# Performance work log

Hardware: AMD Instinct MI355X
Metric: run time of the kernel (lower is better)

The kernel has to match this reference:

```python
import jax, jax.numpy as jnp
import numpy as np

B = 16           # number of graphs
H = 8            # heads
NC = 9           # num_coeffs = (lmax+1)^2
DM = 128         # d_model (sphere_channels)
F = NC * DM      # flat_dim = 1152
HD = F // H      # head_dim = 144
RD = 16          # rope_dim
EPS = 1e-5


def setup_inputs() -> dict:
    key = jax.random.key(0)
    ks = jax.random.split(key, 8)
    N = 8192
    x_emb = jax.random.normal(ks[0], (N, NC, DM), dtype=jnp.float32)
    batch = jnp.sort(jax.random.randint(ks[1], (N,), 0, B)).astype(jnp.int32)
    pos = jax.random.normal(ks[2], (N, 3), dtype=jnp.float32) * 3.0
    Wqkv = jax.random.normal(ks[3], (F, 3 * F), dtype=jnp.float32) / np.sqrt(F)
    Wout = jax.random.normal(ks[4], (F, F), dtype=jnp.float32) / np.sqrt(F)
    rope_freqs = jax.random.normal(ks[5], (RD,), dtype=jnp.float32) * 0.1
    Wrope = jax.random.normal(ks[6], (RD, H), dtype=jnp.float32) / np.sqrt(RD)
    gamma = jnp.ones((F,), dtype=jnp.float32)
    beta = jnp.zeros((F,), dtype=jnp.float32)
    return {"x_emb": x_emb, "pos": pos, "Wqkv": Wqkv, "Wout": Wout,
            "rope_freqs": rope_freqs, "Wrope": Wrope,
            "gamma": gamma, "beta": beta, "batch": batch}


def _pad_layout(batch, N):
    # sorted batch ids -> per-node rank within its graph, sizes per graph
    sizes = jnp.bincount(batch, length=B)                       # [B]
    offsets = jnp.concatenate([jnp.zeros((1,), sizes.dtype), jnp.cumsum(sizes)[:-1]])
    rank = jnp.arange(N, dtype=sizes.dtype) - offsets[batch]    # [N]
    n_max = int(np.asarray(jax.device_get(sizes)).max())        # concrete pad width
    return sizes, rank, n_max


def reference(x_emb, pos, Wqkv, Wout, rope_freqs, Wrope, gamma, beta, batch):
    N = x_emb.shape[0]
    x_flat = x_emb.reshape(N, F)
    sizes, rank, n_max = _pad_layout(batch, N)

    # dense padding  [B, N_max, *]; mask True = padding slot
    x_pad = jnp.zeros((B, n_max, F), x_flat.dtype).at[batch, rank].set(x_flat)
    pos_pad = jnp.zeros((B, n_max, 3), pos.dtype).at[batch, rank].set(pos)
    mask = jnp.arange(n_max)[None, :] >= sizes[:, None]         # [B, N_max]

    qkv = x_pad @ Wqkv                                          # [B, N_max, 3F]
    q, k, v = jnp.split(qkv, 3, axis=-1)
    def heads(t):
        return t.reshape(B, n_max, H, HD).transpose(0, 2, 1, 3)  # [B,H,N_max,HD]
    q, k, v = heads(q), heads(k), heads(v)

    scale = HD ** (-0.5)
    attn = jnp.einsum('bhid,bhjd->bhij', q, k) * scale          # [B,H,N,N]

    # Fourier distance bias
    diff = pos_pad[:, :, None, :] - pos_pad[:, None, :, :]      # [B,N,N,3]
    dist = jnp.linalg.norm(diff, axis=-1)                       # [B,N,N]
    fourier = jnp.cos(dist[..., None] * jnp.abs(rope_freqs))    # [B,N,N,RD]
    bias = jnp.einsum('bijr,rh->bhij', fourier, Wrope)          # [B,H,N,N]
    pad_mask = mask[:, None, :] | mask[:, :, None]              # [B,N,N]
    bias = jnp.where(pad_mask[:, None, :, :], 0.0, bias)
    attn = attn + bias

    attn = jnp.where(mask[:, None, None, :], -jnp.inf, attn)    # key mask
    attn = jax.nn.softmax(attn, axis=-1)
    attn = jnp.nan_to_num(attn)

    out = jnp.einsum('bhij,bhjd->bhid', attn, v)                # [B,H,N,HD]
    out = out.transpose(0, 2, 1, 3).reshape(B, n_max, F) @ Wout
    out_flat = out[batch, rank]                                 # gather back [N,F]

    h = x_flat + out_flat
    mu = jnp.mean(h, axis=-1, keepdims=True)
    var = jnp.var(h, axis=-1, keepdims=True)
    y = (h - mu) / jnp.sqrt(var + EPS) * gamma + beta
    return y.reshape(N, NC, DM)
```

## Files before the change

### kernel.cpp

```cpp
#include <hip/hip_runtime.h>

typedef unsigned short u16;
typedef unsigned int   u32;
typedef __attribute__((ext_vector_type(8)))  __bf16 bf16x8;
typedef __attribute__((ext_vector_type(4)))  float  f32x4;
typedef __attribute__((ext_vector_type(16))) float  f32x16;
typedef __attribute__((ext_vector_type(4)))  u32    u32x4;

#define F_DIM   1152
#define QKV_DIM 3456
#define HD_SCALE 0.083333333333333333f
#define LOG2E    1.4426950408889634f
#define KSC      (HD_SCALE*LOG2E)
#define MAX4    80

static __device__ __forceinline__ u16 f2bf(float f){
    u32 u = __builtin_bit_cast(u32, f);
    u32 r = u + 0x7fffu + ((u >> 16) & 1u);
    return (u16)(r >> 16);
}
static __device__ __forceinline__ u32 cvtpk(float lo, float hi){
    u32 r;
    asm("v_cvt_pk_bf16_f32 %0, %1, %2" : "=v"(r) : "v"(lo), "v"(hi));
    return r;
}

typedef __attribute__((address_space(1))) void gvoid;
typedef __attribute__((address_space(3))) void lvoid;
static __device__ __forceinline__ void gload16(const u16* g, u16* l){
    __builtin_amdgcn_global_load_lds((gvoid*)g, (lvoid*)l, 16, 0, 0);
}

__global__ __launch_bounds__(256) void prep_kernel(
        const float* __restrict__ x, u16* __restrict__ xb, int nCast, int n4,
        const float* __restrict__ Wqkv, u16* __restrict__ wqkvT,
        const float* __restrict__ Wout, u16* __restrict__ woutT,
        const int* __restrict__ batch, int* __restrict__ meta, int N){
    __shared__ float tile[32][33];
    const int b = blockIdx.x, t = threadIdx.x;
    const int T1 = (QKV_DIM/32)*(F_DIM/32);
    const int T2 = (F_DIM/32)*(F_DIM/32);
    if (b < nCast){
        int i = b*256 + t;
        if (i < n4){
            float4 v = ((const float4*)x)[i];
            ((ushort4*)xb)[i] = make_ushort4(f2bf(v.x), f2bf(v.y), f2bf(v.z), f2bf(v.w));
        }
        return;
    }
    if (b < nCast + T1 + T2){
        const float* in; u16* out; int R, C, bi;
        if (b < nCast + T1){ in = Wqkv; out = wqkvT; R = F_DIM; C = QKV_DIM; bi = b - nCast; }
        else               { in = Wout; out = woutT; R = F_DIM; C = F_DIM;  bi = b - nCast - T1; }
        int gx = C/32;
        int c0 = (bi % gx)*32, r0 = (bi / gx)*32;
        int tx = t & 31, ty = t >> 5;
        #pragma unroll
        for (int yy = ty; yy < 32; yy += 8)
            tile[yy][tx] = in[(size_t)(r0+yy)*C + (c0+tx)];
        __syncthreads();
        #pragma unroll
        for (int yy = ty; yy < 32; yy += 8)
            out[(size_t)(c0+yy)*R + (r0+tx)] = f2bf(tile[tx][yy]);
        return;
    }
    if (t <= 16){
        int lo = 0, hi = N;
        while (lo < hi){ int mid = (lo+hi)>>1; if (batch[mid] < t) lo = mid+1; else hi = mid; }
        meta[1+t] = lo;
    }
    __syncthreads();
    if (t == 0){
        int ps = 0, bcnt = 0, cnt4 = 0;
        for (int g = 0; g < 16; g++){
            int ng = meta[2+g] - meta[1+g];
            meta[20+g] = ps;
            meta[40+g] = bcnt;
            int nt = (ng + 31) / 32;
            ps += nt * 32;
            bcnt += nt * nt;
            int nt4 = (nt + 3) / 4;
            for (int q4 = 0; q4 < nt4; q4++){
                meta[64 + cnt4] = g;
                meta[64 + MAX4 + cnt4] = q4;
                cnt4++;
            }
        }
        meta[36] = ps;
        meta[56] = bcnt;
        meta[0]  = cnt4;
    }
}

template<bool OUT_BF16>
__global__ __launch_bounds__(512, 2) void gemm256(const u16* __restrict__ A,
                                                  const u16* __restrict__ Bt,
                                                  void* __restrict__ Cp,
                                                  int M, int Ncols, int K){
    __shared__ u16 sA[4][8192];
    __shared__ u16 sB[4][8192];
    const int nwg = gridDim.x;
    int orig = blockIdx.x;
    int qq = nwg >> 3, rr = nwg & 7;
    int xcd = orig & 7, pos = orig >> 3;
    int nid = (xcd < rr ? xcd*(qq+1) : rr*(qq+1) + (xcd-rr)*qq) + pos;
    const int gx = M >> 8;
    const int bm = (nid % gx) << 8, bn = (nid / gx) << 8;

    const int tid = threadIdx.x;
    const int w = tid >> 6, lane = tid & 63;
    const int wr = w >> 2, wc = w & 3;
    const int fr = lane & 15, fq = lane >> 4;
    const int swz8 = (fq ^ ((fr >> 1) & 3)) * 8;

    const u16* aS[2]; const u16* bS[2]; int dOf[2];
    #pragma unroll
    for (int p = 0; p < 2; p++){
        int idx = p*512 + tid;
        int row = idx >> 2, c = idx & 3;
        int sc = c ^ ((row >> 1) & 3);
        int brow = bn + row; if (brow > Ncols-1) brow = Ncols-1;
        aS[p] = A  + (size_t)(bm + row)*K + sc*8;
        bS[p] = Bt + (size_t)brow*K + sc*8;
        dOf[p] = idx*8;
    }

    f32x4 acc[8][4];
    #pragma unroll
    for (int m = 0; m < 8; m++)
        #pragma unroll
        for (int n = 0; n < 4; n++)
            #pragma unroll
            for (int e = 0; e < 4; e++) acc[m][n][e] = 0.f;

    const int nk = K >> 5;
    #pragma unroll
    for (int p = 0; p < 2; p++){ gload16(aS[p], &sA[0][dOf[p]]); gload16(bS[p], &sB[0][dOf[p]]); }
    #pragma unroll
    for (int p = 0; p < 2; p++){ gload16(aS[p]+32, &sA[1][dOf[p]]); gload16(bS[p]+32, &sB[1][dOf[p]]); }

    #pragma unroll 1
    for (int t = 0; t < nk; t++){
        int tp = (t+2 < nk) ? t+2 : nk-1;
        int bufS = (t+2) & 3;
        #pragma unroll
        for (int p = 0; p < 2; p++){
            gload16(aS[p] + tp*32, &sA[bufS][dOf[p]]);
            gload16(bS[p] + tp*32, &sB[bufS][dOf[p]]);
        }
        asm volatile("s_waitcnt vmcnt(8)\n\ts_barrier" ::: "memory");

        const u16* sAc = &sA[t & 3][0];
        const u16* sBc = &sB[t & 3][0];
        bf16x8 af[8], bfr[4];
        #pragma unroll
        for (int m = 0; m < 8; m++)
            af[m] = *(const bf16x8*)(sAc + (wr*128 + m*16 + fr)*32 + swz8);
        #pragma unroll
        for (int n = 0; n < 4; n++)
            bfr[n] = *(const bf16x8*)(sBc + (wc*64 + n*16 + fr)*32 + swz8);
        __builtin_amdgcn_s_setprio(1);
        #pragma unroll
        for (int m = 0; m < 8; m++)
            #pragma unroll
            for (int n = 0; n < 4; n++)
                acc[m][n] = __builtin_amdgcn_mfma_f32_16x16x32_bf16(af[m], bfr[n], acc[m][n], 0, 0, 0);
        __builtin_amdgcn_s_setprio(0);
    }

    #pragma unroll
    for (int m = 0; m < 8; m++)
        #pragma unroll
        for (int n = 0; n < 4; n++)
            #pragma unroll
            for (int r = 0; r < 4; r++){
                int row = bm + wr*128 + m*16 + fq*4 + r;
                int col = bn + wc*64 + n*16 + fr;
                if (col < Ncols){
                    float v = acc[m][n][r];
                    if (OUT_BF16) ((u16*)Cp)[(size_t)row*Ncols + col] = f2bf(v);
                    else          ((float*)Cp)[(size_t)row*Ncols + col] = v;
                }
            }
}

__global__ __launch_bounds__(256) void pack_v(const u16* __restrict__ qkv,
                                              u16* __restrict__ Vpack,
                                              const int* __restrict__ batch,
                                              const int* __restrict__ meta,
                                              int PT){
    __shared__ u16 tile[32][33];
    int nt0 = blockIdx.x*32, dt0 = blockIdx.y*32, h = blockIdx.z;
    int tx = threadIdx.x & 31, ty = threadIdx.x >> 5;
    #pragma unroll
    for (int yy = ty; yy < 32; yy += 8){
        int node = nt0+yy, d = dt0+tx;
        tile[yy][tx] = (d < 144) ? qkv[(size_t)node*QKV_DIM + 2*F_DIM + h*144 + d] : (u16)0;
    }
    __syncthreads();
    int node = nt0 + tx;
    int g = batch[node];
    int col = meta[20+g] + (node - meta[1+g]);
    int pt = col >> 5, cl = col & 31;
    #pragma unroll
    for (int yy = ty; yy < 32; yy += 8){
        int d = dt0+yy;
        if (d < 144) Vpack[(((size_t)h*PT + pt)*144 + d)*32 + cl] = tile[tx][yy];
    }
}

__global__ __launch_bounds__(256) void bias_kernel(const float* __restrict__ pos,
                                                   const float* __restrict__ rfreq,
                                                   const float* __restrict__ Wrope,
                                                   const int* __restrict__ meta,
                                                   u16* __restrict__ biasP){
    float absf[16], w[16][8];
    #pragma unroll
    for (int r = 0; r < 16; r++){
        absf[r] = fabsf(rfreq[r]);
        #pragma unroll
        for (int h = 0; h < 8; h++) w[r][h] = Wrope[r*8 + h] * LOG2E;
    }
    const int total = meta[56];
    const int t = threadIdx.x;
    for (int bb = blockIdx.x; bb < total; bb += gridDim.x){
        int g = 0;
        while (meta[40 + g + 1] <= bb) g++;
        int rem  = bb - meta[40 + g];
        int goff = meta[1+g];
        int ng   = meta[2+g] - goff;
        int ntg  = (ng + 31) >> 5;
        int qt   = rem / ntg;
        int jt   = rem - qt*ntg;
        size_t base = (size_t)bb * 8192;
        #pragma unroll
        for (int pp = 0; pp < 4; pp++){
            int p = t + pp*256;
            int i = p >> 5, c = p & 31;
            int p4 = c & 15;
            int j  = (p4 & 3) + ((p4 >> 2) << 3) + ((c >> 4) << 2);
            int qn = goff + qt*32 + i;  if (qn >= goff + ng) qn = goff + ng - 1;
            int kn = goff + jt*32 + j;  if (kn >= goff + ng) kn = goff + ng - 1;
            float dx = pos[qn*3+0] - pos[kn*3+0];
            float dy = pos[qn*3+1] - pos[kn*3+1];
            float dz = pos[qn*3+2] - pos[kn*3+2];
            float d  = sqrtf(dx*dx + dy*dy + dz*dz);
            float b[8];
            #pragma unroll
            for (int h = 0; h < 8; h++) b[h] = 0.f;
            #pragma unroll
            for (int r = 0; r < 16; r++){
                float cs = __cosf(d * absf[r]);
                #pragma unroll
                for (int h = 0; h < 8; h++) b[h] = fmaf(cs, w[r][h], b[h]);
            }
            #pragma unroll
            for (int h = 0; h < 8; h++)
                biasP[base + h*1024 + p] = f2bf(b[h]);
        }
    }
}

__global__ __launch_bounds__(256) void attn_kernel(
        const u16* __restrict__ qkv, const u16* __restrict__ Vpack,
        const u16* __restrict__ biasP, u16* __restrict__ attn_out,
        const int* __restrict__ meta, int PT){
    __shared__ u16 sK[2][10240];
    __shared__ u16 sV[2][10240];
    const int h = blockIdx.x & 7, t4 = blockIdx.x >> 3;
    if (t4 >= meta[0]) return;
    const int g    = meta[64 + t4];
    const int q4   = meta[64 + MAX4 + t4];
    const int goff = meta[1+g], gend = meta[2+g];
    const int ng   = gend - goff;
    const int ntg  = (ng + 31) >> 5;
    const int nt2  = (ntg + 1) >> 1;
    const int pst  = meta[20+g];
    const int boffg= meta[40+g];

    const int tid = threadIdx.x;
    const int w = tid >> 6, lane = tid & 63;
    const int li = lane & 31, hi = lane >> 5;
    const int qt = q4*4 + w;
    const int qbase = goff + qt*32;
    const int qtP = (qt < ntg) ? qt : (ntg - 1);

    int kOff[5];
    #pragma unroll
    for (int p = 0; p < 5; p++){
        int idx = p*256 + tid;
        if (idx > 1215) idx = 1215;
        int row = idx/19, c = idx - row*19;
        if (c == 18) c = 0;
        kOff[p] = row*QKV_DIM + c*8;
    }
    const u16* kBase = qkv + (size_t)goff*QKV_DIM + F_DIM + h*144;
    int vOff[5];
    #pragma unroll
    for (int p = 0; p < 5; p++){
        int idx = p*256 + tid;
        if (idx > 1151) idx = 1151;
        int tt = idx/576, i = idx - tt*576;
        int d = i >> 2, c = i & 3;
        vOff[p] = tt*4608 + d*32 + ((c ^ (d & 3)) << 3);
    }
    const u16* vBase = Vpack + ((size_t)h*PT + (pst >> 5))*4608;
    const u16* bBase = biasP + ((size_t)boffg + (size_t)qtP*ntg)*8192 + h*1024 + li*32 + hi*16;

    int qnode = qbase + li; if (qnode >= gend) qnode = gend - 1;
    const u16* qrow = qkv + (size_t)qnode*QKV_DIM + h*144;
    bf16x8 qf[9];
    #pragma unroll
    for (int kk = 0; kk < 9; kk++) qf[kk] = *(const bf16x8*)(qrow + kk*16 + hi*8);

    int jlr[16];
    #pragma unroll
    for (int r = 0; r < 16; r++) jlr[r] = (r & 3) + ((r >> 2) << 3) + (hi << 2);

    float lrun = 0.f;
    f32x16 O[5];
    #pragma unroll
    for (int dt = 0; dt < 5; dt++)
        #pragma unroll
        for (int e = 0; e < 16; e++) O[dt][e] = 0.f;

    u32x4 bA0, bA1, bA2, bA3, bN0, bN1, bN2, bN3;
    {
        int j1 = (ntg > 1) ? 1 : 0;
        bA0 = *(const u32x4*)bBase;
        bA1 = *(const u32x4*)(bBase + 8);
        bA2 = *(const u32x4*)(bBase + (size_t)j1*8192);
        bA3 = *(const u32x4*)(bBase + (size_t)j1*8192 + 8);
        #pragma unroll
        for (int p = 0; p < 5; p++) gload16(kBase + kOff[p], &sK[0][tid*8 + p*2048]);
        #pragma unroll
        for (int p = 0; p < 5; p++) gload16(vBase + vOff[p], &sV[0][tid*8 + p*2048]);
    }
    __syncthreads();

    #pragma unroll 1
    for (int t2 = 0; t2 < nt2; t2++){
        const int cur = t2 & 1;
        int jn0 = 2*t2+2; if (jn0 > ntg-1) jn0 = ntg-1;
        int jn1 = 2*t2+3; if (jn1 > ntg-1) jn1 = ntg-1;
        bN0 = *(const u32x4*)(bBase + (size_t)jn0*8192);
        bN1 = *(const u32x4*)(bBase + (size_t)jn0*8192 + 8);
        bN2 = *(const u32x4*)(bBase + (size_t)jn1*8192);
        bN3 = *(const u32x4*)(bBase + (size_t)jn1*8192 + 8);
        __builtin_amdgcn_sched_barrier(0);
        if (t2+1 < nt2){
            const u16* kb = kBase + (size_t)(t2+1)*64*QKV_DIM;
            const u16* vb = vBase + (size_t)(t2+1)*9216;
            #pragma unroll
            for (int p = 0; p < 5; p++) gload16(kb + kOff[p], &sK[cur^1][tid*8 + p*2048]);
            #pragma unroll
            for (int p = 0; p < 5; p++) gload16(vb + vOff[p], &sV[cur^1][tid*8 + p*2048]);
        }

        const u16* sKc = &sK[cur][0];
        f32x16 saccA, saccB;
        #pragma unroll
        for (int e = 0; e < 16; e++){ saccA[e] = 0.f; saccB[e] = 0.f; }
        __builtin_amdgcn_s_setprio(1);
        #pragma unroll
        for (int kk = 0; kk < 9; kk++){
            bf16x8 kfA = *(const bf16x8*)(sKc + li*152 + kk*16 + hi*8);
            bf16x8 kfB = *(const bf16x8*)(sKc + (32+li)*152 + kk*16 + hi*8);
            saccA = __builtin_amdgcn_mfma_f32_32x32x16_bf16(kfA, qf[kk], saccA, 0, 0, 0);
            saccB = __builtin_amdgcn_mfma_f32_32x32x16_bf16(kfB, qf[kk], saccB, 0, 0, 0);
        }
        __builtin_amdgcn_s_setprio(0);

        float bfA[16], bfB[16];
        #pragma unroll
        for (int q = 0; q < 4; q++){
            bfA[2*q]     = __builtin_bit_cast(float, bA0[q] << 16);
            bfA[2*q+1]   = __builtin_bit_cast(float, bA0[q] & 0xffff0000u);
            bfA[8+2*q]   = __builtin_bit_cast(float, bA1[q] << 16);
            bfA[8+2*q+1] = __builtin_bit_cast(float, bA1[q] & 0xffff0000u);
            bfB[2*q]     = __builtin_bit_cast(float, bA2[q] << 16);
            bfB[2*q+1]   = __builtin_bit_cast(float, bA2[q] & 0xffff0000u);
            bfB[8+2*q]   = __builtin_bit_cast(float, bA3[q] << 16);
            bfB[8+2*q+1] = __builtin_bit_cast(float, bA3[q] & 0xffff0000u);
        }

        const int j0 = t2*64;
        float pA[16], pB[16];
        float psum = 0.f;
        if (j0 + 64 <= ng){
            #pragma unroll
            for (int r = 0; r < 16; r++){
                float sA_ = fminf(fmaf(saccA[r], KSC, bfA[r]), 86.f);
                float sB_ = fminf(fmaf(saccB[r], KSC, bfB[r]), 86.f);
                pA[r] = exp2f(sA_); pB[r] = exp2f(sB_);
                psum += pA[r] + pB[r];
            }
        } else {
            #pragma unroll
            for (int r = 0; r < 16; r++){
                float sA_ = fminf(fmaf(saccA[r], KSC, bfA[r]), 86.f);
                float sB_ = fminf(fmaf(saccB[r], KSC, bfB[r]), 86.f);
                pA[r] = (j0 + jlr[r]      < ng) ? exp2f(sA_) : 0.f;
                pB[r] = (j0 + 32 + jlr[r] < ng) ? exp2f(sB_) : 0.f;
                psum += pA[r] + pB[r];
            }
        }
        psum += __shfl_xor(psum, 32);
        lrun += psum;

        u32 cA[8], oA[8], cB[8], oB[8];
        #pragma unroll
        for (int q = 0; q < 8; q++){ cA[q] = cvtpk(pA[2*q], pA[2*q+1]);
                                     cB[q] = cvtpk(pB[2*q], pB[2*q+1]); }
        #pragma unroll
        for (int q = 0; q < 8; q++){ oA[q] = (u32)__shfl_xor((int)cA[q], 32);
                                     oB[q] = (u32)__shfl_xor((int)cB[q], 32); }
        u32x4 a0, a1, b0, b1;
        if (hi == 0){
            a0[0]=cA[0]; a0[1]=cA[1]; a0[2]=oA[0]; a0[3]=oA[1];
            a1[0]=cA[4]; a1[1]=cA[5]; a1[2]=oA[4]; a1[3]=oA[5];
            b0[0]=cB[0]; b0[1]=cB[1]; b0[2]=oB[0]; b0[3]=oB[1];
            b1[0]=cB[4]; b1[1]=cB[5]; b1[2]=oB[4]; b1[3]=oB[5];
        } else {
            a0[0]=oA[2]; a0[1]=oA[3]; a0[2]=cA[2]; a0[3]=cA[3];
            a1[0]=oA[6]; a1[1]=oA[7]; a1[2]=cA[6]; a1[3]=cA[7];
            b0[0]=oB[2]; b0[1]=oB[3]; b0[2]=cB[2]; b0[3]=cB[3];
            b1[0]=oB[6]; b1[1]=oB[7]; b1[2]=cB[6]; b1[3]=cB[7];
        }
        bf16x8 pafA0 = __builtin_bit_cast(bf16x8, a0);
        bf16x8 pafA1 = __builtin_bit_cast(bf16x8, a1);
        bf16x8 pafB0 = __builtin_bit_cast(bf16x8, b0);
        bf16x8 pafB1 = __builtin_bit_cast(bf16x8, b1);

        const u16* sVc = &sV[cur][0];
        __builtin_amdgcn_s_setprio(1);
        #pragma unroll
        for (int dt = 0; dt < 5; dt++){
            int d = dt*32 + li;
            int dc = (d > 143) ? 143 : d;
            int swzlo = ((hi     ^ (dc & 3)) << 3);
            int swzhi = (((2+hi) ^ (dc & 3)) << 3);
            bf16x8 vA0 = *(const bf16x8*)(sVc + dc*32 + swzlo);
            bf16x8 vA1 = *(const bf16x8*)(sVc + dc*32 + swzhi);
            bf16x8 vB0 = *(const bf16x8*)(sVc + 4608 + dc*32 + swzlo);
            bf16x8 vB1 = *(const bf16x8*)(sVc + 4608 + dc*32 + swzhi);
            O[dt] = __builtin_amdgcn_mfma_f32_32x32x16_bf16(pafA0, vA0, O[dt], 0, 0, 0);
            O[dt] = __builtin_amdgcn_mfma_f32_32x32x16_bf16(pafA1, vA1, O[dt], 0, 0, 0);
            O[dt] = __builtin_amdgcn_mfma_f32_32x32x16_bf16(pafB0, vB0, O[dt], 0, 0, 0);
            O[dt] = __builtin_amdgcn_mfma_f32_32x32x16_bf16(pafB1, vB1, O[dt], 0, 0, 0);
        }
        __builtin_amdgcn_s_setprio(0);

        bA0 = bN0; bA1 = bN1; bA2 = bN2; bA3 = bN3;
        __syncthreads();
    }

    if (qt < ntg){
        float lr[16];
        #pragma unroll
        for (int r = 0; r < 16; r++) lr[r] = 1.0f / __shfl(lrun, jlr[r]);
        #pragma unroll
        for (int dt = 0; dt < 5; dt++){
            int d = dt*32 + li;
            if (d < 144){
                #pragma unroll
                for (int r = 0; r < 16; r++){
                    int qi = jlr[r];
                    if (qt*32 + qi < ng)
                        attn_out[(size_t)(qbase + qi)*F_DIM + h*144 + d] = f2bf(O[dt][r]*lr[r]);
                }
            }
        }
    }
}

__global__ __launch_bounds__(256) void ln_kernel(const float* __restrict__ x,
                                                 float* __restrict__ io,
                                                 const float* __restrict__ gamma,
                                                 const float* __restrict__ beta){
    const int node = blockIdx.x;
    const float* xr = x  + (size_t)node*F_DIM;
    float* yr       = io + (size_t)node*F_DIM;
    const int t = threadIdx.x;
    float h[5]; float s = 0.f, ss = 0.f;
    #pragma unroll
    for (int i = 0; i < 5; i++){
        int idx = t + i*256;
        float v = 0.f;
        if (idx < F_DIM) v = xr[idx] + yr[idx];
        h[i] = v; s += v; ss += v*v;
    }
    #pragma unroll
    for (int o = 32; o > 0; o >>= 1){ s += __shfl_down(s, o); ss += __shfl_down(ss, o); }
    __shared__ float rs[4], rss[4];
    __shared__ float smu, srstd;
    if ((t & 63) == 0){ rs[t>>6] = s; rss[t>>6] = ss; }
    __syncthreads();
    if (t == 0){
        float S  = rs[0]+rs[1]+rs[2]+rs[3];
        float SS = rss[0]+rss[1]+rss[2]+rss[3];
        float mu = S * (1.f/F_DIM);
        float var = SS * (1.f/F_DIM) - mu*mu;
        smu = mu; srstd = rsqrtf(var + 1e-5f);
    }
    __syncthreads();
    float mu = smu, rstd = srstd;
    #pragma unroll
    for (int i = 0; i < 5; i++){
        int idx = t + i*256;
        if (idx < F_DIM) yr[idx] = (h[i]-mu)*rstd*gamma[idx] + beta[idx];
    }
}

extern "C" void kernel_launch(void* const* d_in, const int* in_sizes, int n_in,
                              void* d_out, int out_size, void* d_ws, size_t ws_size,
                              hipStream_t stream){
    const float* x     = (const float*)d_in[0];
    const float* pos   = (const float*)d_in[1];
    const float* Wqkv  = (const float*)d_in[2];
    const float* Wout  = (const float*)d_in[3];
    const float* rfreq = (const float*)d_in[4];
    const float* Wrope = (const float*)d_in[5];
    const float* gamma = (const float*)d_in[6];
    const float* beta  = (const float*)d_in[7];
    const int*   batch = (const int*)d_in[8];

    const int N  = in_sizes[0] / F_DIM;
    const int PN = N + 512;
    const int PT = PN / 32;

    char* ws = (char*)d_ws;
    size_t off = 0;
    auto alloc = [&](size_t b){ size_t o = off; off += (b + 255) & ~(size_t)255; return o; };
    int* meta   = (int*)(ws + alloc((size_t)(64 + 2*MAX4 + 64)*sizeof(int)));
    u16* xb     = (u16*)(ws + alloc((size_t)N*F_DIM*2));
    u16* wqkvT  = (u16*)(ws + alloc((size_t)QKV_DIM*F_DIM*2));
    u16* woutT  = (u16*)(ws + alloc((size_t)F_DIM*F_DIM*2));
    u16* qkv    = (u16*)(ws + alloc((size_t)N*QKV_DIM*2));
    u16* Vpack  = (u16*)(ws + alloc((size_t)8*PT*144*32*2));
    u16* biasb  = (u16*)(ws + off);
    (void)ws_size; (void)n_in; (void)out_size;

    const int n4    = N*F_DIM/4;
    const int nCast = (n4 + 255)/256;
    const int nT    = (QKV_DIM/32)*(F_DIM/32) + (F_DIM/32)*(F_DIM/32);
    hipLaunchKernelGGL(prep_kernel, dim3(nCast + nT + 1), dim3(256), 0, stream,
                       x, xb, nCast, n4, Wqkv, wqkvT, Wout, woutT, batch, meta, N);
    hipLaunchKernelGGL((gemm256<true>), dim3((N/256)*((QKV_DIM+255)/256)), dim3(512), 0, stream,
                       xb, wqkvT, (void*)qkv, N, QKV_DIM, F_DIM);
    hipLaunchKernelGGL(pack_v, dim3(N/32, 5, 8), dim3(256), 0, stream,
                       qkv, Vpack, batch, meta, PT);
    hipLaunchKernelGGL(bias_kernel, dim3(2048), dim3(256), 0, stream,
                       pos, rfreq, Wrope, meta, biasb);
    hipLaunchKernelGGL(attn_kernel, dim3(MAX4*8), dim3(256), 0, stream,
                       qkv, Vpack, biasb, xb, meta, PT);
    hipLaunchKernelGGL((gemm256<false>), dim3((N/256)*((F_DIM+255)/256)), dim3(512), 0, stream,
                       xb, woutT, d_out, N, F_DIM, F_DIM);
    hipLaunchKernelGGL(ln_kernel, dim3(N), dim3(256), 0, stream,
                       x, (float*)d_out, gamma, beta);
}
```

Before: 301.2 us.

## Fuse bias computation into prep kernel and halve attention key tile

Moves the Fourier distance bias computation into the prep kernel as an extra 2048 blocks, which recompute graph offsets locally, and removes the separate bias launch. The bias work then runs alongside the cast and transpose work. The attention kernel now processes one 32-key tile per iteration instead of two, which shrinks shared memory and registers to allow higher occupancy. The trade-off is more loop iterations and barriers per key and less MFMA work between syncs.

```diff
diff --git a/kernel.cpp b/kernel.cpp
--- a/kernel.cpp
+++ b/kernel.cpp
@@ -13,6 +13,7 @@
 #define LOG2E    1.4426950408889634f
 #define KSC      (HD_SCALE*LOG2E)
 #define MAX4    80
+#define BIAS_BLKS 2048
 
 static __device__ __forceinline__ u16 f2bf(float f){
     u32 u = __builtin_bit_cast(u32, f);
@@ -35,23 +36,93 @@
         const float* __restrict__ x, u16* __restrict__ xb, int nCast, int n4,
         const float* __restrict__ Wqkv, u16* __restrict__ wqkvT,
         const float* __restrict__ Wout, u16* __restrict__ woutT,
+        const float* __restrict__ pos, const float* __restrict__ rfreq,
+        const float* __restrict__ Wrope, u16* __restrict__ biasP,
         const int* __restrict__ batch, int* __restrict__ meta, int N){
     __shared__ float tile[32][33];
+    __shared__ int goffs[17];
+    __shared__ int bpre[17];
     const int b = blockIdx.x, t = threadIdx.x;
     const int T1 = (QKV_DIM/32)*(F_DIM/32);
     const int T2 = (F_DIM/32)*(F_DIM/32);
-    if (b < nCast){
-        int i = b*256 + t;
+
+    if (b < BIAS_BLKS){
+        if (t <= 16){
+            int lo = 0, hi = N;
+            while (lo < hi){ int mid = (lo+hi)>>1; if (batch[mid] < t) lo = mid+1; else hi = mid; }
+            goffs[t] = lo;
+        }
+        __syncthreads();
+        if (t == 0){
+            int bc = 0;
+            for (int g = 0; g < 16; g++){
+                bpre[g] = bc;
+                int ng = goffs[g+1] - goffs[g];
+                int ntg = (ng + 31) >> 5;
+                bc += ntg*ntg;
+            }
+            bpre[16] = bc;
+        }
+        __syncthreads();
+        float absf[16], w[16][8];
+        #pragma unroll
+        for (int r = 0; r < 16; r++){
+            absf[r] = fabsf(rfreq[r]);
+            #pragma unroll
+            for (int h = 0; h < 8; h++) w[r][h] = Wrope[r*8 + h] * LOG2E;
+        }
+        const int total = bpre[16];
+        for (int bb = b; bb < total; bb += BIAS_BLKS){
+            int g = 0;
+            while (bpre[g+1] <= bb) g++;
+            int rem  = bb - bpre[g];
+            int goff = goffs[g];
+            int ng   = goffs[g+1] - goff;
+            int ntg  = (ng + 31) >> 5;
+            int qt   = rem / ntg;
+            int jt   = rem - qt*ntg;
+            size_t base = (size_t)bb * 8192;
+            #pragma unroll
+            for (int pp = 0; pp < 4; pp++){
+                int p = t + pp*256;
+                int i = p >> 5, c = p & 31;
+                int p4 = c & 15;
+                int j  = (p4 & 3) + ((p4 >> 2) << 3) + ((c >> 4) << 2);
+                int qn = goff + qt*32 + i;  if (qn >= goff + ng) qn = goff + ng - 1;
+                int kn = goff + jt*32 + j;  if (kn >= goff + ng) kn = goff + ng - 1;
+                float dx = pos[qn*3+0] - pos[kn*3+0];
+                float dy = pos[qn*3+1] - pos[kn*3+1];
+                float dz = pos[qn*3+2] - pos[kn*3+2];
+                float d  = sqrtf(dx*dx + dy*dy + dz*dz);
+                float bv[8];
+                #pragma unroll
+                for (int h = 0; h < 8; h++) bv[h] = 0.f;
+                #pragma unroll
+                for (int r = 0; r < 16; r++){
+                    float cs = __cosf(d * absf[r]);
+                    #pragma unroll
+                    for (int h = 0; h < 8; h++) bv[h] = fmaf(cs, w[r][h], bv[h]);
+                }
+                #pragma unroll
+                for (int h = 0; h < 8; h++)
+                    biasP[base + h*1024 + p] = f2bf(bv[h]);
+            }
+        }
+        return;
+    }
+    const int b2 = b - BIAS_BLKS;
+    if (b2 < nCast){
+        int i = b2*256 + t;
         if (i < n4){
             float4 v = ((const float4*)x)[i];
             ((ushort4*)xb)[i] = make_ushort4(f2bf(v.x), f2bf(v.y), f2bf(v.z), f2bf(v.w));
         }
         return;
     }
-    if (b < nCast + T1 + T2){
+    if (b2 < nCast + T1 + T2){
         const float* in; u16* out; int R, C, bi;
-        if (b < nCast + T1){ in = Wqkv; out = wqkvT; R = F_DIM; C = QKV_DIM; bi = b - nCast; }
-        else               { in = Wout; out = woutT; R = F_DIM; C = F_DIM;  bi = b - nCast - T1; }
+        if (b2 < nCast + T1){ in = Wqkv; out = wqkvT; R = F_DIM; C = QKV_DIM; bi = b2 - nCast; }
+        else                { in = Wout; out = woutT; R = F_DIM; C = F_DIM;  bi = b2 - nCast - T1; }
         int gx = C/32;
         int c0 = (bi % gx)*32, r0 = (bi / gx)*32;
         int tx = t & 31, ty = t >> 5;
@@ -209,64 +280,12 @@
     }
 }
 
-__global__ __launch_bounds__(256) void bias_kernel(const float* __restrict__ pos,
-                                                   const float* __restrict__ rfreq,
-                                                   const float* __restrict__ Wrope,
-                                                   const int* __restrict__ meta,
-                                                   u16* __restrict__ biasP){
-    float absf[16], w[16][8];
-    #pragma unroll
-    for (int r = 0; r < 16; r++){
-        absf[r] = fabsf(rfreq[r]);
-        #pragma unroll
-        for (int h = 0; h < 8; h++) w[r][h] = Wrope[r*8 + h] * LOG2E;
-    }
-    const int total = meta[56];
-    const int t = threadIdx.x;
-    for (int bb = blockIdx.x; bb < total; bb += gridDim.x){
-        int g = 0;
-        while (meta[40 + g + 1] <= bb) g++;
-        int rem  = bb - meta[40 + g];
-        int goff = meta[1+g];
-        int ng   = meta[2+g] - goff;
-        int ntg  = (ng + 31) >> 5;
-        int qt   = rem / ntg;
-        int jt   = rem - qt*ntg;
-        size_t base = (size_t)bb * 8192;
-        #pragma unroll
-        for (int pp = 0; pp < 4; pp++){
-            int p = t + pp*256;
-            int i = p >> 5, c = p & 31;
-            int p4 = c & 15;
-            int j  = (p4 & 3) + ((p4 >> 2) << 3) + ((c >> 4) << 2);
-            int qn = goff + qt*32 + i;  if (qn >= goff + ng) qn = goff + ng - 1;
-            int kn = goff + jt*32 + j;  if (kn >= goff + ng) kn = goff + ng - 1;
-            float dx = pos[qn*3+0] - pos[kn*3+0];
-            float dy = pos[qn*3+1] - pos[kn*3+1];
-            float dz = pos[qn*3+2] - pos[kn*3+2];
-            float d  = sqrtf(dx*dx + dy*dy + dz*dz);
-            float b[8];
-            #pragma unroll
-            for (int h = 0; h < 8; h++) b[h] = 0.f;
-            #pragma unroll
-            for (int r = 0; r < 16; r++){
-                float cs = __cosf(d * absf[r]);
-                #pragma unroll
-                for (int h = 0; h < 8; h++) b[h] = fmaf(cs, w[r][h], b[h]);
-            }
-            #pragma unroll
-            for (int h = 0; h < 8; h++)
-                biasP[base + h*1024 + p] = f2bf(b[h]);
-        }
-    }
-}
-
 __global__ __launch_bounds__(256) void attn_kernel(
         const u16* __restrict__ qkv, const u16* __restrict__ Vpack,
         const u16* __restrict__ biasP, u16* __restrict__ attn_out,
         const int* __restrict__ meta, int PT){
-    __shared__ u16 sK[2][10240];
-    __shared__ u16 sV[2][10240];
+    __shared__ u16 sK[2][4864];
+    __shared__ u16 sV[2][4608];
     const int h = blockIdx.x & 7, t4 = blockIdx.x >> 3;
     if (t4 >= meta[0]) return;
     const int g    = meta[64 + t4];
@@ -274,7 +293,6 @@
     const int goff = meta[1+g], gend = meta[2+g];
     const int ng   = gend - goff;
     const int ntg  = (ng + 31) >> 5;
-    const int nt2  = (ntg + 1) >> 1;
     const int pst  = meta[20+g];
     const int boffg= meta[40+g];
 
@@ -285,24 +303,23 @@
     const int qbase = goff + qt*32;
     const int qtP = (qt < ntg) ? qt : (ntg - 1);
 
-    int kOff[5];
-    #pragma unroll
-    for (int p = 0; p < 5; p++){
+    int kOff[3];
+    #pragma unroll
+    for (int p = 0; p < 3; p++){
         int idx = p*256 + tid;
-        if (idx > 1215) idx = 1215;
+        if (idx > 607) idx = 607;
         int row = idx/19, c = idx - row*19;
         if (c == 18) c = 0;
         kOff[p] = row*QKV_DIM + c*8;
     }
     const u16* kBase = qkv + (size_t)goff*QKV_DIM + F_DIM + h*144;
-    int vOff[5];
-    #pragma unroll
-    for (int p = 0; p < 5; p++){
+    int vOff[3];
+    #pragma unroll
+    for (int p = 0; p < 3; p++){
         int idx = p*256 + tid;
-        if (idx > 1151) idx = 1151;
-        int tt = idx/576, i = idx - tt*576;
-        int d = i >> 2, c = i & 3;
-        vOff[p] = tt*4608 + d*32 + ((c ^ (d & 3)) << 3);
+        if (idx > 575) idx = 575;
+        int d = idx >> 2, c = idx & 3;
+        vOff[p] = d*32 + ((c ^ (d & 3)) << 3);
     }
     const u16* vBase = Vpack + ((size_t)h*PT + (pst >> 5))*4608;
     const u16* bBase = biasP + ((size_t)boffg + (size_t)qtP*ntg)*8192 + h*1024 + li*32 + hi*16;
@@ -324,113 +341,93 @@
         #pragma unroll
         for (int e = 0; e < 16; e++) O[dt][e] = 0.f;
 
-    u32x4 bA0, bA1, bA2, bA3, bN0, bN1, bN2, bN3;
+    u32x4 bA0, bA1, bN0, bN1;
+    bA0 = *(const u32x4*)bBase;
+    bA1 = *(const u32x4*)(bBase + 8);
     {
-        int j1 = (ntg > 1) ? 1 : 0;
-        bA0 = *(const u32x4*)bBase;
-        bA1 = *(const u32x4*)(bBase + 8);
-        bA2 = *(const u32x4*)(bBase + (size_t)j1*8192);
-        bA3 = *(const u32x4*)(bBase + (size_t)j1*8192 + 8);
-        #pragma unroll
-        for (int p = 0; p < 5; p++) gload16(kBase + kOff[p], &sK[0][tid*8 + p*2048]);
-        #pragma unroll
-        for (int p = 0; p < 5; p++) gload16(vBase + vOff[p], &sV[0][tid*8 + p*2048]);
+        gload16(kBase + kOff[0], &sK[0][tid*8]);
+        gload16(kBase + kOff[1], &sK[0][(256+tid)*8]);
+        if (tid < 96) gload16(kBase + kOff[2], &sK[0][(512+tid)*8]);
+        gload16(vBase + vOff[0], &sV[0][tid*8]);
+        gload16(vBase + vOff[1], &sV[0][(256+tid)*8]);
+        if (tid < 64) gload16(vBase + vOff[2], &sV[0][(512+tid)*8]);
     }
     __syncthreads();
 
     #pragma unroll 1
-    for (int t2 = 0; t2 < nt2; t2++){
-        const int cur = t2 & 1;
-        int jn0 = 2*t2+2; if (jn0 > ntg-1) jn0 = ntg-1;
-        int jn1 = 2*t2+3; if (jn1 > ntg-1) jn1 = ntg-1;
-        bN0 = *(const u32x4*)(bBase + (size_t)jn0*8192);
-        bN1 = *(const u32x4*)(bBase + (size_t)jn0*8192 + 8);
-        bN2 = *(const u32x4*)(bBase + (size_t)jn1*8192);
-        bN3 = *(const u32x4*)(bBase + (size_t)jn1*8192 + 8);
+    for (int t = 0; t < ntg; t++){
+        const int cur = t & 1;
+        int tn = (t+1 < ntg) ? t+1 : ntg-1;
+        bN0 = *(const u32x4*)(bBase + (size_t)tn*8192);
+        bN1 = *(const u32x4*)(bBase + (size_t)tn*8192 + 8);
         __builtin_amdgcn_sched_barrier(0);
-        if (t2+1 < nt2){
-            const u16* kb = kBase + (size_t)(t2+1)*64*QKV_DIM;
-            const u16* vb = vBase + (size_t)(t2+1)*9216;
-            #pragma unroll
-            for (int p = 0; p < 5; p++) gload16(kb + kOff[p], &sK[cur^1][tid*8 + p*2048]);
-            #pragma unroll
-            for (int p = 0; p < 5; p++) gload16(vb + vOff[p], &sV[cur^1][tid*8 + p*2048]);
+        if (t+1 < ntg){
+            const u16* kb = kBase + (size_t)(t+1)*32*QKV_DIM;
+            const u16* vb = vBase + (size_t)(t+1)*4608;
+            gload16(kb + kOff[0], &sK[cur^1][tid*8]);
+            gload16(kb + kOff[1], &sK[cur^1][(256+tid)*8]);
+            if (tid < 96) gload16(kb + kOff[2], &sK[cur^1][(512+tid)*8]);
+            gload16(vb + vOff[0], &sV[cur^1][tid*8]);
+            gload16(vb + vOff[1], &sV[cur^1][(256+tid)*8]);
+            if (tid < 64) gload16(vb + vOff[2], &sV[cur^1][(512+tid)*8]);
         }
 
         const u16* sKc = &sK[cur][0];
-        f32x16 saccA, saccB;
-        #pragma unroll
-        for (int e = 0; e < 16; e++){ saccA[e] = 0.f; saccB[e] = 0.f; }
+        f32x16 sacc;
+        #pragma unroll
+        for (int e = 0; e < 16; e++) sacc[e] = 0.f;
         __builtin_amdgcn_s_setprio(1);
         #pragma unroll
         for (int kk = 0; kk < 9; kk++){
-            bf16x8 kfA = *(const bf16x8*)(sKc + li*152 + kk*16 + hi*8);
-            bf16x8 kfB = *(const bf16x8*)(sKc + (32+li)*152 + kk*16 + hi*8);
-            saccA = __builtin_amdgcn_mfma_f32_32x32x16_bf16(kfA, qf[kk], saccA, 0, 0, 0);
-            saccB = __builtin_amdgcn_mfma_f32_32x32x16_bf16(kfB, qf[kk], saccB, 0, 0, 0);
+            bf16x8 kf = *(const bf16x8*)(sKc + li*152 + kk*16 + hi*8);
+            sacc = __builtin_amdgcn_mfma_f32_32x32x16_bf16(kf, qf[kk], sacc, 0, 0, 0);
         }
         __builtin_amdgcn_s_setprio(0);
 
-        float bfA[16], bfB[16];
+        float bfv[16];
         #pragma unroll
         for (int q = 0; q < 4; q++){
-            bfA[2*q]     = __builtin_bit_cast(float, bA0[q] << 16);
-            bfA[2*q+1]   = __builtin_bit_cast(float, bA0[q] & 0xffff0000u);
-            bfA[8+2*q]   = __builtin_bit_cast(float, bA1[q] << 16);
-            bfA[8+2*q+1] = __builtin_bit_cast(float, bA1[q] & 0xffff0000u);
-            bfB[2*q]     = __builtin_bit_cast(float, bA2[q] << 16);
-            bfB[2*q+1]   = __builtin_bit_cast(float, bA2[q] & 0xffff0000u);
-            bfB[8+2*q]   = __builtin_bit_cast(float, bA3[q] << 16);
-            bfB[8+2*q+1] = __builtin_bit_cast(float, bA3[q] & 0xffff0000u);
-        }
-
-        const int j0 = t2*64;
-        float pA[16], pB[16];
+            bfv[2*q]     = __builtin_bit_cast(float, bA0[q] << 16);
+            bfv[2*q+1]   = __builtin_bit_cast(float, bA0[q] & 0xffff0000u);
+            bfv[8+2*q]   = __builtin_bit_cast(float, bA1[q] << 16);
+            bfv[8+2*q+1] = __builtin_bit_cast(float, bA1[q] & 0xffff0000u);
+        }
+
+        const int j0 = t*32;
+        float p[16];
         float psum = 0.f;
-        if (j0 + 64 <= ng){
+        if (j0 + 32 <= ng){
             #pragma unroll
             for (int r = 0; r < 16; r++){
-                float sA_ = fminf(fmaf(saccA[r], KSC, bfA[r]), 86.f);
-                float sB_ = fminf(fmaf(saccB[r], KSC, bfB[r]), 86.f);
-                pA[r] = exp2f(sA_); pB[r] = exp2f(sB_);
-                psum += pA[r] + pB[r];
+                float s_ = fminf(fmaf(sacc[r], KSC, bfv[r]), 86.f);
+                p[r] = exp2f(s_); psum += p[r];
             }
         } else {
             #pragma unroll
             for (int r = 0; r < 16; r++){
-                float sA_ = fminf(fmaf(saccA[r], KSC, bfA[r]), 86.f);
-                float sB_ = fminf(fmaf(saccB[r], KSC, bfB[r]), 86.f);
-                pA[r] = (j0 + jlr[r]      < ng) ? exp2f(sA_) : 0.f;
-                pB[r] = (j0 + 32 + jlr[r] < ng) ? exp2f(sB_) : 0.f;
-                psum += pA[r] + pB[r];
+                float s_ = fminf(fmaf(sacc[r], KSC, bfv[r]), 86.f);
+                p[r] = (j0 + jlr[r] < ng) ? exp2f(s_) : 0.f;
+                psum += p[r];
             }
         }
         psum += __shfl_xor(psum, 32);
         lrun += psum;
 
-        u32 cA[8], oA[8], cB[8], oB[8];
-        #pragma unroll
-        for (int q = 0; q < 8; q++){ cA[q] = cvtpk(pA[2*q], pA[2*q+1]);
-                                     cB[q] = cvtpk(pB[2*q], pB[2*q+1]); }
-        #pragma unroll
-        for (int q = 0; q < 8; q++){ oA[q] = (u32)__shfl_xor((int)cA[q], 32);
-                                     oB[q] = (u32)__shfl_xor((int)cB[q], 32); }
-        u32x4 a0, a1, b0, b1;
+        u32 cpk[8], opk[8];
+        #pragma unroll
+        for (int q = 0; q < 8; q++) cpk[q] = cvtpk(p[2*q], p[2*q+1]);
+        #pragma unroll
+        for (int q = 0; q < 8; q++) opk[q] = (u32)__shfl_xor((int)cpk[q], 32);
+        u32x4 a0, a1;
         if (hi == 0){
-            a0[0]=cA[0]; a0[1]=cA[1]; a0[2]=oA[0]; a0[3]=oA[1];
-            a1[0]=cA[4]; a1[1]=cA[5]; a1[2]=oA[4]; a1[3]=oA[5];
-            b0[0]=cB[0]; b0[1]=cB[1]; b0[2]=oB[0]; b0[3]=oB[1];
-            b1[0]=cB[4]; b1[1]=cB[5]; b1[2]=oB[4]; b1[3]=oB[5];
+            a0[0]=cpk[0]; a0[1]=cpk[1]; a0[2]=opk[0]; a0[3]=opk[1];
+            a1[0]=cpk[4]; a1[1]=cpk[5]; a1[2]=opk[4]; a1[3]=opk[5];
         } else {
-            a0[0]=oA[2]; a0[1]=oA[3]; a0[2]=cA[2]; a0[3]=cA[3];
-            a1[0]=oA[6]; a1[1]=oA[7]; a1[2]=cA[6]; a1[3]=cA[7];
-            b0[0]=oB[2]; b0[1]=oB[3]; b0[2]=cB[2]; b0[3]=cB[3];
-            b1[0]=oB[6]; b1[1]=oB[7]; b1[2]=cB[6]; b1[3]=cB[7];
-        }
-        bf16x8 pafA0 = __builtin_bit_cast(bf16x8, a0);
-        bf16x8 pafA1 = __builtin_bit_cast(bf16x8, a1);
-        bf16x8 pafB0 = __builtin_bit_cast(bf16x8, b0);
-        bf16x8 pafB1 = __builtin_bit_cast(bf16x8, b1);
+            a0[0]=opk[2]; a0[1]=opk[3]; a0[2]=cpk[2]; a0[3]=cpk[3];
+            a1[0]=opk[6]; a1[1]=opk[7]; a1[2]=cpk[6]; a1[3]=cpk[7];
+        }
+        bf16x8 paf0 = __builtin_bit_cast(bf16x8, a0);
+        bf16x8 paf1 = __builtin_bit_cast(bf16x8, a1);
 
         const u16* sVc = &sV[cur][0];
         __builtin_amdgcn_s_setprio(1);
@@ -440,18 +437,14 @@
             int dc = (d > 143) ? 143 : d;
             int swzlo = ((hi     ^ (dc & 3)) << 3);
             int swzhi = (((2+hi) ^ (dc & 3)) << 3);
-            bf16x8 vA0 = *(const bf16x8*)(sVc + dc*32 + swzlo);
-            bf16x8 vA1 = *(const bf16x8*)(sVc + dc*32 + swzhi);
-            bf16x8 vB0 = *(const bf16x8*)(sVc + 4608 + dc*32 + swzlo);
-            bf16x8 vB1 = *(const bf16x8*)(sVc + 4608 + dc*32 + swzhi);
-            O[dt] = __builtin_amdgcn_mfma_f32_32x32x16_bf16(pafA0, vA0, O[dt], 0, 0, 0);
-            O[dt] = __builtin_amdgcn_mfma_f32_32x32x16_bf16(pafA1, vA1, O[dt], 0, 0, 0);
-            O[dt] = __builtin_amdgcn_mfma_f32_32x32x16_bf16(pafB0, vB0, O[dt], 0, 0, 0);
-            O[dt] = __builtin_amdgcn_mfma_f32_32x32x16_bf16(pafB1, vB1, O[dt], 0, 0, 0);
+            bf16x8 v0 = *(const bf16x8*)(sVc + dc*32 + swzlo);
+            bf16x8 v1 = *(const bf16x8*)(sVc + dc*32 + swzhi);
+            O[dt] = __builtin_amdgcn_mfma_f32_32x32x16_bf16(paf0, v0, O[dt], 0, 0, 0);
+            O[dt] = __builtin_amdgcn_mfma_f32_32x32x16_bf16(paf1, v1, O[dt], 0, 0, 0);
         }
         __builtin_amdgcn_s_setprio(0);
 
-        bA0 = bN0; bA1 = bN1; bA2 = bN2; bA3 = bN3;
+        bA0 = bN0; bA1 = bN1;
         __syncthreads();
     }
 
@@ -544,14 +537,13 @@
     const int n4    = N*F_DIM/4;
     const int nCast = (n4 + 255)/256;
     const int nT    = (QKV_DIM/32)*(F_DIM/32) + (F_DIM/32)*(F_DIM/32);
-    hipLaunchKernelGGL(prep_kernel, dim3(nCast + nT + 1), dim3(256), 0, stream,
-                       x, xb, nCast, n4, Wqkv, wqkvT, Wout, woutT, batch, meta, N);
+    hipLaunchKernelGGL(prep_kernel, dim3(BIAS_BLKS + nCast + nT + 1), dim3(256), 0, stream,
+                       x, xb, nCast, n4, Wqkv, wqkvT, Wout, woutT,
+                       pos, rfreq, Wrope, biasb, batch, meta, N);
     hipLaunchKernelGGL((gemm256<true>), dim3((N/256)*((QKV_DIM+255)/256)), dim3(512), 0, stream,
                        xb, wqkvT, (void*)qkv, N, QKV_DIM, F_DIM);
     hipLaunchKernelGGL(pack_v, dim3(N/32, 5, 8), dim3(256), 0, stream,
                        qkv, Vpack, batch, meta, PT);
-    hipLaunchKernelGGL(bias_kernel, dim3(2048), dim3(256), 0, stream,
-                       pos, rfreq, Wrope, meta, biasb);
     hipLaunchKernelGGL(attn_kernel, dim3(MAX4*8), dim3(256), 0, stream,
                        qkv, Vpack, biasb, xb, meta, PT);
     hipLaunchKernelGGL((gemm256<false>), dim3((N/256)*((F_DIM+255)/256)), dim3(512), 0, stream,
```

After: 287.5 us. 4.5% less time.
